# Optimization experiments

Measured on AMD Instinct MI355X. Metric: run time of the kernel, lower is better.

## Reference

```python
import jax, jax.numpy as jnp
import numpy as np

N = 100000      # number of 1-simplices (edges of the power grid)
NNZ = 3200000   # nonzeros in L1_tilde (avg degree 32)
CIN = 128
COUT = 128
BN_EPS = 1e-5


def setup_inputs() -> dict:
    key = jax.random.key(0)
    ks = jax.random.split(key, 8)
    Z_H = jax.random.normal(ks[0], (N, CIN), dtype=jnp.float32)
    rows = jax.random.randint(ks[1], (NNZ,), 0, N)
    cols = jax.random.randint(ks[2], (NNZ,), 0, N)
    values = jax.random.normal(ks[3], (NNZ,), dtype=jnp.float32)
    # nn.Linear params (Kaiming-ish scale)
    W = jax.random.normal(ks[4], (CIN, COUT), dtype=jnp.float32) / np.float32(np.sqrt(CIN))
    b = jnp.zeros((COUT,), dtype=jnp.float32)
    # BatchNorm1d affine params
    gamma = jnp.ones((COUT,), dtype=jnp.float32)
    beta = jnp.zeros((COUT,), dtype=jnp.float32)
    return {"Z_H": Z_H, "values": values, "W": W, "b": b,
            "gamma": gamma, "beta": beta, "rows": rows, "cols": cols}


def reference(Z_H, values, W, b, gamma, beta, rows, cols):
    # Linear projection: [N, CIN] @ [CIN, COUT] + [COUT]
    Z_theta = Z_H @ W + b
    # Sparse Laplacian matmul (COO SpMM): Z_conv[r] += v * Z_theta[c]
    gathered = values[:, None] * Z_theta[cols]          # [NNZ, COUT]
    Z_conv = jax.ops.segment_sum(gathered, rows, num_segments=Z_H.shape[0])
    # BatchNorm1d (training mode: biased batch stats over the node dim)
    mean = jnp.mean(Z_conv, axis=0)
    var = jnp.var(Z_conv, axis=0)
    Z_bn = (Z_conv - mean) * (gamma / jnp.sqrt(var + BN_EPS)) + beta
    # ReLU + row-wise max pool -> [N, 1]
    Z_psi = jax.nn.relu(Z_bn)
    return jnp.max(Z_psi, axis=1, keepdims=True)
```

## Files before the change

### kernel.cpp

```cpp
#include <hip/hip_runtime.h>
#include <hip/hip_bf16.h>

#define CIN  128
#define COUT 128
#define BN_EPS 1e-5f
#define RPB   64
#define MAXNB 2048
#define PCHUNK 8192
#define CAP   2560
#define GB    512

typedef __attribute__((ext_vector_type(8))) short short8;
typedef __attribute__((ext_vector_type(4))) float f32x4;

__device__ __forceinline__ unsigned short f2bf(float f) {
    unsigned u = __float_as_uint(f);
    u += 0x7fffu + ((u >> 16) & 1u);
    return (unsigned short)(u >> 16);
}

__device__ __forceinline__ void gemm_body(
    const float* __restrict__ Z, const float* __restrict__ W,
    const float* __restrict__ b, unsigned short* __restrict__ Zt,
    int N, int bid)
{
    const int lane = threadIdx.x & 63;
    const int wid  = threadIdx.x >> 6;
    const int lm   = lane & 15;
    const int lg   = lane >> 4;

    short8 bfr[4][8];
#pragma unroll
    for (int kc = 0; kc < 4; ++kc) {
#pragma unroll
        for (int ct = 0; ct < 8; ++ct) {
            union { short8 v; unsigned short u[8]; } bf;
#pragma unroll
            for (int e = 0; e < 8; ++e)
                bf.u[e] = f2bf(W[(kc * 32 + lg * 8 + e) * COUT + ct * 16 + lm]);
            bfr[kc][ct] = bf.v;
        }
    }

    float bias[8];
#pragma unroll
    for (int ct = 0; ct < 8; ++ct) bias[ct] = b[ct * 16 + lm];

    const int ntiles = (N + 63) / 64;
    for (int tile = bid; tile < ntiles; tile += GB) {
        const int row0 = tile * 64 + wid * 16;
        if (row0 >= N) continue;

        const int arow = row0 + lm;
        const bool aval = arow < N;
        const float* zrow = Z + (size_t)arow * CIN;

        f32x4 acc[8];
#pragma unroll
        for (int ct = 0; ct < 8; ++ct) {
            f32x4 a = {bias[ct], bias[ct], bias[ct], bias[ct]};
            acc[ct] = a;
        }

#pragma unroll
        for (int kc = 0; kc < 4; ++kc) {
            union { short8 v; unsigned short u[8]; } af;
            if (aval) {
                const float4 z0 = *((const float4*)(zrow + kc * 32 + lg * 8));
                const float4 z1 = *((const float4*)(zrow + kc * 32 + lg * 8 + 4));
                af.u[0] = f2bf(z0.x); af.u[1] = f2bf(z0.y);
                af.u[2] = f2bf(z0.z); af.u[3] = f2bf(z0.w);
                af.u[4] = f2bf(z1.x); af.u[5] = f2bf(z1.y);
                af.u[6] = f2bf(z1.z); af.u[7] = f2bf(z1.w);
            } else {
#pragma unroll
                for (int e = 0; e < 8; ++e) af.u[e] = 0;
            }
#pragma unroll
            for (int ct = 0; ct < 8; ++ct)
                acc[ct] = __builtin_amdgcn_mfma_f32_16x16x32_bf16(
                    af.v, bfr[kc][ct], acc[ct], 0, 0, 0);
        }

#pragma unroll
        for (int i = 0; i < 4; ++i) {
            const int grow = row0 + lg * 4 + i;
            if (grow < N) {
#pragma unroll
                for (int ct = 0; ct < 8; ++ct)
                    Zt[(size_t)grow * COUT + ct * 16 + lm] = f2bf(acc[ct][i]);
            }
        }
    }
}

__device__ __forceinline__ void partition_body(
    const int* __restrict__ rows, const int* __restrict__ cols,
    const float* __restrict__ vals, int* __restrict__ bucketCur,
    uint2* __restrict__ ebuck, int nnz, int NB, int pb)
{
    __shared__ int h[MAXNB];
    __shared__ int basecur[MAXNB];
    const int t = threadIdx.x;

    for (int i = t; i < NB; i += 256) h[i] = 0;
    __syncthreads();

    const int c0 = pb * PCHUNK;
    const int ce = min(c0 + PCHUNK, nnz);

    int rloc[PCHUNK / 256];
#pragma unroll
    for (int j = 0; j < PCHUNK / 256; ++j) {
        const int i = c0 + j * 256 + t;
        int r = -1;
        if (i < ce) r = rows[i];
        rloc[j] = r;
        if (r >= 0) atomicAdd(&h[r >> 6], 1);
    }
    __syncthreads();

    for (int i = t; i < NB; i += 256) {
        const int c = h[i];
        basecur[i] = c ? (i * CAP + atomicAdd(&bucketCur[i], c)) : 0;
    }
    __syncthreads();

#pragma unroll
    for (int j = 0; j < PCHUNK / 256; ++j) {
        const int i = c0 + j * 256 + t;
        const int r = rloc[j];
        if (r >= 0) {
            const int p = atomicAdd(&basecur[r >> 6], 1);
            ebuck[p] = make_uint2((unsigned)cols[i] | ((unsigned)(r & (RPB - 1)) << 17),
                                  __float_as_uint(vals[i]));
        }
    }
}

__global__ __launch_bounds__(256, 2) void gemm_part_kernel(
    const float* __restrict__ Z, const float* __restrict__ W,
    const float* __restrict__ b, unsigned short* __restrict__ Zt,
    const int* __restrict__ rows, const int* __restrict__ cols,
    const float* __restrict__ vals, int* __restrict__ bucketCur,
    uint2* __restrict__ ebuck, int nnz, int N, int NB)
{
    if (blockIdx.x < GB) {
        gemm_body(Z, W, b, Zt, N, blockIdx.x);
    } else {
        partition_body(rows, cols, vals, bucketCur, ebuck, nnz, NB, blockIdx.x - GB);
    }
}

__global__ __launch_bounds__(256) void bucket_build_kernel(
    const uint2* __restrict__ ebuck, const int* __restrict__ bucketCur,
    uint2* __restrict__ epack, uint2* __restrict__ rowinfo, int N)
{
    __shared__ int cnt[RPB];
    __shared__ int sc[RPB];
    __shared__ int loc[RPB];

    const int b    = blockIdx.x;
    const int base = b * CAP;
    const int count = bucketCur[b];
    const int t = threadIdx.x;

    if (t < RPB) cnt[t] = 0;
    __syncthreads();

    for (int i = t; i < count; i += 256)
        atomicAdd(&cnt[ebuck[base + i].x >> 17], 1);
    __syncthreads();

    if (t < RPB) sc[t] = cnt[t];
    __syncthreads();
#pragma unroll
    for (int off = 1; off < RPB; off <<= 1) {
        int v = 0;
        if (t < RPB && t >= off) v = sc[t - off];
        __syncthreads();
        if (t < RPB) sc[t] += v;
        __syncthreads();
    }

    if (t < RPB) {
        const int start = sc[t] - cnt[t];
        loc[t] = start;
        const int row = b * RPB + t;
        if (row < N) rowinfo[row] = make_uint2((unsigned)(base + start), (unsigned)cnt[t]);
    }
    __syncthreads();

    for (int i = t; i < count; i += 256) {
        const uint2 e = ebuck[base + i];
        const int rl  = (int)(e.x >> 17);
        const int pos = atomicAdd(&loc[rl], 1);
        epack[base + pos] = make_uint2(e.x & 0x1FFFFu, e.y);
    }
}

__global__ __launch_bounds__(256) void gather_kernel(
    const unsigned short* __restrict__ Zt, const uint2* __restrict__ epack,
    const uint2* __restrict__ rowinfo, unsigned int* __restrict__ Zc,
    float* __restrict__ stats, int N)
{
    __shared__ float sbuf[256];
    sbuf[threadIdx.x] = 0.f;
    __syncthreads();

    const int wid  = threadIdx.x >> 6;
    const int lane = threadIdx.x & 63;
    const int eo   = lane >> 5;
    const int cg   = lane & 31;

    float s0 = 0.f, s1 = 0.f, s2 = 0.f, s3 = 0.f;
    float q0 = 0.f, q1 = 0.f, q2 = 0.f, q3 = 0.f;

    for (int row = blockIdx.x * 4 + wid; row < N; row += gridDim.x * 4) {
        const uint2 ri = rowinfo[row];
        const int beg = (int)ri.x;
        const int end = beg + (int)ri.y;

        float a0 = 0.f, a1 = 0.f, a2 = 0.f, a3 = 0.f;

        int i = beg + eo;
        for (; i + 6 < end; i += 8) {
            const uint2 p0 = epack[i];
            const uint2 p1 = epack[i + 2];
            const uint2 p2 = epack[i + 4];
            const uint2 p3 = epack[i + 6];
            const uint2 g0 = *((const uint2*)(Zt + (size_t)p0.x * COUT + cg * 4));
            const uint2 g1 = *((const uint2*)(Zt + (size_t)p1.x * COUT + cg * 4));
            const uint2 g2 = *((const uint2*)(Zt + (size_t)p2.x * COUT + cg * 4));
            const uint2 g3 = *((const uint2*)(Zt + (size_t)p3.x * COUT + cg * 4));
            const float v0 = __uint_as_float(p0.y);
            const float v1 = __uint_as_float(p1.y);
            const float v2 = __uint_as_float(p2.y);
            const float v3 = __uint_as_float(p3.y);
            a0 = fmaf(v0, __uint_as_float(g0.x << 16), a0);
            a1 = fmaf(v0, __uint_as_float(g0.x & 0xffff0000u), a1);
            a2 = fmaf(v0, __uint_as_float(g0.y << 16), a2);
            a3 = fmaf(v0, __uint_as_float(g0.y & 0xffff0000u), a3);
            a0 = fmaf(v1, __uint_as_float(g1.x << 16), a0);
            a1 = fmaf(v1, __uint_as_float(g1.x & 0xffff0000u), a1);
            a2 = fmaf(v1, __uint_as_float(g1.y << 16), a2);
            a3 = fmaf(v1, __uint_as_float(g1.y & 0xffff0000u), a3);
            a0 = fmaf(v2, __uint_as_float(g2.x << 16), a0);
            a1 = fmaf(v2, __uint_as_float(g2.x & 0xffff0000u), a1);
            a2 = fmaf(v2, __uint_as_float(g2.y << 16), a2);
            a3 = fmaf(v2, __uint_as_float(g2.y & 0xffff0000u), a3);
            a0 = fmaf(v3, __uint_as_float(g3.x << 16), a0);
            a1 = fmaf(v3, __uint_as_float(g3.x & 0xffff0000u), a1);
            a2 = fmaf(v3, __uint_as_float(g3.y << 16), a2);
            a3 = fmaf(v3, __uint_as_float(g3.y & 0xffff0000u), a3);
        }
        for (; i < end; i += 2) {
            const uint2 p = epack[i];
            const uint2 g = *((const uint2*)(Zt + (size_t)p.x * COUT + cg * 4));
            const float vp = __uint_as_float(p.y);
            a0 = fmaf(vp, __uint_as_float(g.x << 16), a0);
            a1 = fmaf(vp, __uint_as_float(g.x & 0xffff0000u), a1);
            a2 = fmaf(vp, __uint_as_float(g.y << 16), a2);
            a3 = fmaf(vp, __uint_as_float(g.y & 0xffff0000u), a3);
        }

        a0 += __shfl_xor(a0, 32);
        a1 += __shfl_xor(a1, 32);
        a2 += __shfl_xor(a2, 32);
        a3 += __shfl_xor(a3, 32);

        if (eo == 0) {
            uint2 o;
            o.x = (unsigned)f2bf(a0) | ((unsigned)f2bf(a1) << 16);
            o.y = (unsigned)f2bf(a2) | ((unsigned)f2bf(a3) << 16);
            *((uint2*)(Zc + (size_t)row * (COUT / 2) + cg * 2)) = o;
            s0 += a0; s1 += a1; s2 += a2; s3 += a3;
            q0 = fmaf(a0, a0, q0);
            q1 = fmaf(a1, a1, q1);
            q2 = fmaf(a2, a2, q2);
            q3 = fmaf(a3, a3, q3);
        }
    }

    if (eo == 0) {
        const int c0 = cg * 4;
        atomicAdd(&sbuf[c0 + 0], s0);
        atomicAdd(&sbuf[c0 + 1], s1);
        atomicAdd(&sbuf[c0 + 2], s2);
        atomicAdd(&sbuf[c0 + 3], s3);
        atomicAdd(&sbuf[128 + c0 + 0], q0);
        atomicAdd(&sbuf[128 + c0 + 1], q1);
        atomicAdd(&sbuf[128 + c0 + 2], q2);
        atomicAdd(&sbuf[128 + c0 + 3], q3);
    }
    __syncthreads();
    atomicAdd(&stats[threadIdx.x], sbuf[threadIdx.x]);
}

__global__ __launch_bounds__(256) void finalize_kernel(
    const unsigned int* __restrict__ Zc, const float* __restrict__ stats,
    const float* __restrict__ gamma, const float* __restrict__ beta,
    float* __restrict__ out, int N)
{
    const int row = blockIdx.x * 4 + (threadIdx.x >> 6);
    if (row >= N) return;
    const int lane = threadIdx.x & 63;
    const int c0 = lane * 2;

    const unsigned g = Zc[(size_t)row * (COUT / 2) + lane];
    const float x0 = __uint_as_float(g << 16);
    const float x1 = __uint_as_float(g & 0xffff0000u);

    const float invN = 1.0f / (float)N;
    const float m0 = stats[c0] * invN;
    const float m1 = stats[c0 + 1] * invN;
    const float v0 = stats[128 + c0] * invN - m0 * m0;
    const float v1 = stats[128 + c0 + 1] * invN - m1 * m1;
    const float sc0 = gamma[c0]     * rsqrtf(v0 + BN_EPS);
    const float sc1 = gamma[c0 + 1] * rsqrtf(v1 + BN_EPS);

    float y0 = (x0 - m0) * sc0 + beta[c0];
    float y1 = (x1 - m1) * sc1 + beta[c0 + 1];
    y0 = fmaxf(y0, 0.f);
    y1 = fmaxf(y1, 0.f);

    float mx = fmaxf(y0, y1);
#pragma unroll
    for (int off = 32; off > 0; off >>= 1)
        mx = fmaxf(mx, __shfl_xor(mx, off));

    if (lane == 0) out[row] = mx;
}

extern "C" void kernel_launch(void* const* d_in, const int* in_sizes, int n_in,
                              void* d_out, int out_size, void* d_ws, size_t ws_size,
                              hipStream_t stream)
{
    const float* Z_H   = (const float*)d_in[0];
    const float* vals  = (const float*)d_in[1];
    const float* W     = (const float*)d_in[2];
    const float* b     = (const float*)d_in[3];
    const float* gamma = (const float*)d_in[4];
    const float* beta  = (const float*)d_in[5];
    const int*   rows  = (const int*)d_in[6];
    const int*   cols  = (const int*)d_in[7];
    float* out = (float*)d_out;

    const int N   = in_sizes[0] / CIN;
    const int nnz = in_sizes[1];
    const int NB  = (N + RPB - 1) / RPB;
    const int pblocks = (nnz + PCHUNK - 1) / PCHUNK;

    char* ws = (char*)d_ws;
    size_t off = 0;
    unsigned short* Zt = (unsigned short*)(ws + off); off += (size_t)N * COUT * sizeof(unsigned short);
    unsigned int*   Zc = (unsigned int*)(ws + off);   off += (size_t)N * (COUT / 2) * sizeof(unsigned int);
    uint2* ebuck  = (uint2*)(ws + off);  off += (size_t)NB * CAP * sizeof(uint2);
    uint2* epack  = (uint2*)(ws + off);  off += (size_t)NB * CAP * sizeof(uint2);
    uint2* rowinfo = (uint2*)(ws + off); off += (size_t)N * sizeof(uint2);
    int* bucketCur = (int*)(ws + off);   off += (size_t)NB * sizeof(int);
    float* stats   = (float*)(ws + off); off += 256 * sizeof(float);

    hipMemsetAsync(bucketCur, 0, ((size_t)NB + 256) * sizeof(int), stream);

    gemm_part_kernel<<<GB + pblocks, 256, 0, stream>>>(
        Z_H, W, b, Zt, rows, cols, vals, bucketCur, ebuck, nnz, N, NB);

    bucket_build_kernel<<<NB, 256, 0, stream>>>(ebuck, bucketCur, epack, rowinfo, N);

    gather_kernel<<<2048, 256, 0, stream>>>(Zt, epack, rowinfo, Zc, stats, N);

    finalize_kernel<<<(N + 3) / 4, 256, 0, stream>>>(Zc, stats, gamma, beta, out, N);
}
```

Measured before the change: 271.8 us.

## Fuse bucket build into gather via shared-memory CSR per 64-row bucket

Merges the bucket-sort kernel and the SpMM gather kernel into one: each block loads its bucket's edges into registers, counting-sorts them by local row into shared memory, then gathers directly from that shared buffer. This removes the global epack/rowinfo round trip and one kernel launch. It also reorders the combined gemm/partition kernel so that partition blocks come first. In exchange it uses about 20KB of LDS per block, which may lower occupancy, and the gather grid becomes one block per bucket (about 1563) instead of a grid-stride loop.

```diff
diff --git a/kernel.cpp b/kernel.cpp
--- a/kernel.cpp
+++ b/kernel.cpp
@@ -143,92 +143,95 @@
     const float* __restrict__ b, unsigned short* __restrict__ Zt,
     const int* __restrict__ rows, const int* __restrict__ cols,
     const float* __restrict__ vals, int* __restrict__ bucketCur,
-    uint2* __restrict__ ebuck, int nnz, int N, int NB)
-{
-    if (blockIdx.x < GB) {
-        gemm_body(Z, W, b, Zt, N, blockIdx.x);
+    uint2* __restrict__ ebuck, int nnz, int N, int NB, int pblocks)
+{
+    if ((int)blockIdx.x < pblocks) {
+        partition_body(rows, cols, vals, bucketCur, ebuck, nnz, NB, blockIdx.x);
     } else {
-        partition_body(rows, cols, vals, bucketCur, ebuck, nnz, NB, blockIdx.x - GB);
-    }
-}
-
-__global__ __launch_bounds__(256) void bucket_build_kernel(
-    const uint2* __restrict__ ebuck, const int* __restrict__ bucketCur,
-    uint2* __restrict__ epack, uint2* __restrict__ rowinfo, int N)
+        gemm_body(Z, W, b, Zt, N, blockIdx.x - pblocks);
+    }
+}
+
+__global__ __launch_bounds__(256) void gather_build_kernel(
+    const unsigned short* __restrict__ Zt, const uint2* __restrict__ ebuck,
+    const int* __restrict__ bucketCur, unsigned int* __restrict__ Zc,
+    float* __restrict__ stats, int N)
 {
     __shared__ int cnt[RPB];
-    __shared__ int sc[RPB];
+    __shared__ int scn[RPB];
     __shared__ int loc[RPB];
-
-    const int b    = blockIdx.x;
+    __shared__ uint2 ebuf[CAP];
+    __shared__ float sbuf[256];
+
+    const int t = threadIdx.x;
+    const int b = blockIdx.x;
     const int base = b * CAP;
-    const int count = bucketCur[b];
-    const int t = threadIdx.x;
-
+    int count = bucketCur[b];
+    if (count > CAP) count = CAP;
+
+    sbuf[t] = 0.f;
     if (t < RPB) cnt[t] = 0;
     __syncthreads();
 
-    for (int i = t; i < count; i += 256)
-        atomicAdd(&cnt[ebuck[base + i].x >> 17], 1);
-    __syncthreads();
-
-    if (t < RPB) sc[t] = cnt[t];
+    uint2 er[CAP / 256];
+#pragma unroll
+    for (int j = 0; j < CAP / 256; ++j) {
+        const int i = j * 256 + t;
+        if (i < count) {
+            er[j] = ebuck[base + i];
+            atomicAdd(&cnt[er[j].x >> 17], 1);
+        }
+    }
+    __syncthreads();
+
+    if (t < RPB) scn[t] = cnt[t];
     __syncthreads();
 #pragma unroll
     for (int off = 1; off < RPB; off <<= 1) {
         int v = 0;
-        if (t < RPB && t >= off) v = sc[t - off];
+        if (t < RPB && t >= off) v = scn[t - off];
         __syncthreads();
-        if (t < RPB) sc[t] += v;
+        if (t < RPB) scn[t] += v;
         __syncthreads();
     }
-
-    if (t < RPB) {
-        const int start = sc[t] - cnt[t];
-        loc[t] = start;
-        const int row = b * RPB + t;
-        if (row < N) rowinfo[row] = make_uint2((unsigned)(base + start), (unsigned)cnt[t]);
-    }
-    __syncthreads();
-
-    for (int i = t; i < count; i += 256) {
-        const uint2 e = ebuck[base + i];
-        const int rl  = (int)(e.x >> 17);
-        const int pos = atomicAdd(&loc[rl], 1);
-        epack[base + pos] = make_uint2(e.x & 0x1FFFFu, e.y);
-    }
-}
-
-__global__ __launch_bounds__(256) void gather_kernel(
-    const unsigned short* __restrict__ Zt, const uint2* __restrict__ epack,
-    const uint2* __restrict__ rowinfo, unsigned int* __restrict__ Zc,
-    float* __restrict__ stats, int N)
-{
-    __shared__ float sbuf[256];
-    sbuf[threadIdx.x] = 0.f;
-    __syncthreads();
-
-    const int wid  = threadIdx.x >> 6;
-    const int lane = threadIdx.x & 63;
+    if (t < RPB) loc[t] = scn[t] - cnt[t];
+    __syncthreads();
+
+#pragma unroll
+    for (int j = 0; j < CAP / 256; ++j) {
+        const int i = j * 256 + t;
+        if (i < count) {
+            const uint2 e = er[j];
+            const int rl  = (int)(e.x >> 17);
+            const int pos = atomicAdd(&loc[rl], 1);
+            ebuf[pos] = make_uint2(e.x & 0x1FFFFu, e.y);
+        }
+    }
+    __syncthreads();
+
+    const int wid  = t >> 6;
+    const int lane = t & 63;
     const int eo   = lane >> 5;
     const int cg   = lane & 31;
 
     float s0 = 0.f, s1 = 0.f, s2 = 0.f, s3 = 0.f;
     float q0 = 0.f, q1 = 0.f, q2 = 0.f, q3 = 0.f;
 
-    for (int row = blockIdx.x * 4 + wid; row < N; row += gridDim.x * 4) {
-        const uint2 ri = rowinfo[row];
-        const int beg = (int)ri.x;
-        const int end = beg + (int)ri.y;
+    const int row0 = b * RPB;
+    for (int r = wid; r < RPB; r += 4) {
+        const int row = row0 + r;
+        if (row >= N) break;
+        const int end = scn[r];
+        const int beg = end - cnt[r];
 
         float a0 = 0.f, a1 = 0.f, a2 = 0.f, a3 = 0.f;
 
         int i = beg + eo;
         for (; i + 6 < end; i += 8) {
-            const uint2 p0 = epack[i];
-            const uint2 p1 = epack[i + 2];
-            const uint2 p2 = epack[i + 4];
-            const uint2 p3 = epack[i + 6];
+            const uint2 p0 = ebuf[i];
+            const uint2 p1 = ebuf[i + 2];
+            const uint2 p2 = ebuf[i + 4];
+            const uint2 p3 = ebuf[i + 6];
             const uint2 g0 = *((const uint2*)(Zt + (size_t)p0.x * COUT + cg * 4));
             const uint2 g1 = *((const uint2*)(Zt + (size_t)p1.x * COUT + cg * 4));
             const uint2 g2 = *((const uint2*)(Zt + (size_t)p2.x * COUT + cg * 4));
@@ -255,7 +258,7 @@
             a3 = fmaf(v3, __uint_as_float(g3.y & 0xffff0000u), a3);
         }
         for (; i < end; i += 2) {
-            const uint2 p = epack[i];
+            const uint2 p = ebuf[i];
             const uint2 g = *((const uint2*)(Zt + (size_t)p.x * COUT + cg * 4));
             const float vp = __uint_as_float(p.y);
             a0 = fmaf(vp, __uint_as_float(g.x << 16), a0);
@@ -294,7 +297,7 @@
         atomicAdd(&sbuf[128 + c0 + 3], q3);
     }
     __syncthreads();
-    atomicAdd(&stats[threadIdx.x], sbuf[threadIdx.x]);
+    atomicAdd(&stats[t], sbuf[t]);
 }
 
 __global__ __launch_bounds__(256) void finalize_kernel(
@@ -356,19 +359,15 @@
     unsigned short* Zt = (unsigned short*)(ws + off); off += (size_t)N * COUT * sizeof(unsigned short);
     unsigned int*   Zc = (unsigned int*)(ws + off);   off += (size_t)N * (COUT / 2) * sizeof(unsigned int);
     uint2* ebuck  = (uint2*)(ws + off);  off += (size_t)NB * CAP * sizeof(uint2);
-    uint2* epack  = (uint2*)(ws + off);  off += (size_t)NB * CAP * sizeof(uint2);
-    uint2* rowinfo = (uint2*)(ws + off); off += (size_t)N * sizeof(uint2);
     int* bucketCur = (int*)(ws + off);   off += (size_t)NB * sizeof(int);
     float* stats   = (float*)(ws + off); off += 256 * sizeof(float);
 
     hipMemsetAsync(bucketCur, 0, ((size_t)NB + 256) * sizeof(int), stream);
 
-    gemm_part_kernel<<<GB + pblocks, 256, 0, stream>>>(
-        Z_H, W, b, Zt, rows, cols, vals, bucketCur, ebuck, nnz, N, NB);
-
-    bucket_build_kernel<<<NB, 256, 0, stream>>>(ebuck, bucketCur, epack, rowinfo, N);
-
-    gather_kernel<<<2048, 256, 0, stream>>>(Zt, epack, rowinfo, Zc, stats, N);
+    gemm_part_kernel<<<pblocks + GB, 256, 0, stream>>>(
+        Z_H, W, b, Zt, rows, cols, vals, bucketCur, ebuck, nnz, N, NB, pblocks);
+
+    gather_build_kernel<<<NB, 256, 0, stream>>>(Zt, ebuck, bucketCur, Zc, stats, N);
 
     finalize_kernel<<<(N + 3) / 4, 256, 0, stream>>>(Zc, stats, gamma, beta, out, N);
 }
```

Result: faster. 245.7 us (median of 2 runs) (-9.6%).
